# Kernel optimization log

Hardware: AMD Instinct MI355X
Metric: run time of the kernel (lower is better)

The kernel has to match this reference:

```python
import jax, jax.numpy as jnp
import numpy as np
from jax import lax

T_DATA = 20000
E_NO = 2000
I_NO = 500
SUB_NO = 16
SYN_B = 3
HID = 256
T_SYN = 200
T_ENC = 80


def _causal_conv(x, kern):
    # x: [T, S] per-subunit drive; kern: [S, K] causal kernels (index = lag)
    S, K = kern.shape
    lhs = jnp.pad(x.T, ((0, 0), (K - 1, 0)))[None]        # [1, S, T+K-1]
    rhs = kern[:, ::-1][:, None, :]                        # flip then correlate == torch conv1d path
    out = lax.conv_general_dilated(lhs, rhs, (1,), 'VALID', feature_group_count=S)
    return out[0].T                                        # [T, S]


def setup_inputs() -> dict:
    key = jax.random.key(0)
    ks = jax.random.split(key, 16)
    V_in = jax.random.normal(ks[0], (T_DATA,), jnp.float32) * 5.0 - 69.0
    S_e = jax.random.bernoulli(ks[1], 0.02, (T_DATA, E_NO)).astype(jnp.float32)
    S_i = jax.random.bernoulli(ks[2], 0.02, (T_DATA, I_NO)).astype(jnp.float32)
    # synapse -> subunit one-hot assignment matrices [sub_no, n_syn]
    C_syn_e = jax.nn.one_hot(jax.random.randint(ks[3], (E_NO,), 0, SUB_NO), SUB_NO, dtype=jnp.float32).T
    C_syn_i = jax.nn.one_hot(jax.random.randint(ks[4], (I_NO,), 0, SUB_NO), SUB_NO, dtype=jnp.float32).T
    # parameters, initialized exactly as in __init__
    K_syn = jnp.stack([jnp.full((SUB_NO, SYN_B), 0.04),
                       jnp.full((SUB_NO, SYN_B), -0.02),
                       jnp.full((SUB_NO, SYN_B), 0.02)], axis=-1)          # [sub, B, 3]
    tau_syn = jnp.tile((jnp.arange(SYN_B, dtype=jnp.float32) + 1.6)[:, None], (1, 3))  # [B, 3]
    delta_syn = jnp.full((SUB_NO, 2), 2.0, jnp.float32)
    enc_bias = jnp.zeros((SUB_NO - 1,), jnp.float32)
    W_in = 2 * T_ENC - 1

    def lin(k, fan_out, fan_in):
        kw, kb = jax.random.split(k)
        s = 1.0 / np.sqrt(fan_in)
        return (jax.random.uniform(kw, (fan_out, fan_in), jnp.float32, -s, s),
                jax.random.uniform(kb, (fan_out,), jnp.float32, -s, s))

    W1, b1 = lin(ks[5], HID, W_in)
    W2, b2 = lin(ks[6], HID, HID)
    W3, b3 = lin(ks[7], HID, HID)
    W4, b4 = lin(ks[8], SUB_NO - 1, HID)
    a1 = jnp.float32(0.25)
    a2 = jnp.float32(0.25)
    a3 = jnp.float32(0.25)
    return dict(V_in=V_in, S_e=S_e, S_i=S_i, C_syn_e=C_syn_e, C_syn_i=C_syn_i,
                K_syn=K_syn, tau_syn=tau_syn, delta_syn=delta_syn, enc_bias=enc_bias,
                W1=W1, b1=b1, a1=a1, W2=W2, b2=b2, a2=a2, W3=W3, b3=b3, a3=a3,
                W4=W4, b4=b4)


def reference(V_in, S_e, S_i, C_syn_e, C_syn_i, K_syn, tau_syn, delta_syn, enc_bias,
              W1, b1, a1, W2, b2, a2, W3, b3, a3, W4, b4):
    T = V_in.shape[0]
    # ---- spike_convolve, fully vectorized over (subunit, basis) ----
    t = jnp.arange(T_SYN, dtype=V_in.dtype)                 # [T_syn]
    d = jnp.exp(delta_syn)                                   # [sub, 2]
    te = jnp.maximum(t[None, :] - d[:, 0:1], 0.0)            # [sub, T_syn]
    ti = jnp.maximum(t[None, :] - d[:, 1:2], 0.0)
    tau = jnp.exp(tau_syn)                                   # [B, 3]
    tte = te[:, None, :] / tau[None, :, 0, None]             # [sub, B, T_syn]
    tti = ti[:, None, :] / tau[None, :, 1, None]
    ker_e = jnp.einsum('sbt,sb->st', tte * jnp.exp(-tte), K_syn[:, :, 0])
    ker_i = jnp.einsum('sbt,sb->st', tti * jnp.exp(-tti), K_syn[:, :, 1])
    in_e = S_e @ C_syn_e.T                                   # [T, sub]
    in_i = S_i @ C_syn_i.T
    S_conv = _causal_conv(in_e, ker_e) + _causal_conv(in_i, ker_i)   # [T, sub]
    # ---- encode: batched sliding-window MLP (replaces per-timestep loop) ----
    W = 2 * T_ENC - 1
    Vpad = jnp.zeros((T + W,), V_in.dtype).at[T_ENC - 1:T_ENC - 1 + T].set(V_in)
    idx = jnp.arange(T)[:, None] + jnp.arange(W)[None, :]    # [T, W]
    win = Vpad[idx]                                          # [T, W]
    prelu = lambda x, a: jnp.where(x >= 0, x, a * x)
    h = prelu(win @ W1.T + b1, a1)
    h = prelu(h @ W2.T + b2, a2)
    h = prelu(h @ W3.T + b3, a3)
    nn_out = h @ W4.T + b4                                   # [T, sub-1]
    return jax.nn.sigmoid(nn_out + S_conv[:, 1:] + enc_bias)
```

## Files before the change

kernel.cpp:

```cpp
#include <hip/hip_runtime.h>
#include <cstdint>
#include <cstddef>

#define T_DATA 20000
#define E_NO 2000
#define I_NO 500
#define SUB_NO 16
#define HID 256
#define T_SYN 200
#define T_ENC 80
#define W_IN 159

typedef __attribute__((ext_vector_type(8))) __bf16 bf16x8;
typedef __attribute__((ext_vector_type(8))) short short8;
typedef __attribute__((ext_vector_type(4))) float floatx4;
typedef __attribute__((ext_vector_type(4))) unsigned int uint4v;
typedef __attribute__((ext_vector_type(2))) unsigned int uint2v;

__device__ __forceinline__ float bf2f(unsigned short u) {
    union { unsigned int i; float f; } v; v.i = ((unsigned int)u) << 16; return v.f;
}
__device__ __forceinline__ unsigned short f2bf(float f) {
    union { float f; unsigned int i; } v; v.f = f;
    unsigned int r = v.i + 0x7FFFu + ((v.i >> 16) & 1u);
    return (unsigned short)(r >> 16);
}
__device__ __forceinline__ float inload(const void* p, int i, int isbf) {
    return isbf ? bf2f(((const unsigned short*)p)[i]) : ((const float*)p)[i];
}

__device__ __forceinline__ int detect_bf(const void* Se, int* sfl) {
    if (threadIdx.x == 0) *sfl = 0;
    __syncthreads();
    const unsigned int* w = (const unsigned int*)Se;
    int la = 0;
    #pragma unroll
    for (int i = 0; i < 4; i++)
        la |= (w[i * 256 + threadIdx.x] & 0xFFFFu) ? 1 : 0;
    if (la) atomicOr(sfl, 1);
    __syncthreads();
    return *sfl;
}

#define OFF_KERE   16u
#define OFF_KERI   12816u
#define OFF_SHE    25616u
#define OFF_SHI    33616u
#define OFF_W1H    35616u
#define OFF_W1L    117536u
#define OFF_W2H    199456u
#define OFF_W2L    330528u
#define OFF_W3H    461600u
#define OFF_W3L    592672u
#define OFF_W4H    723744u
#define OFF_W4L    731936u
#define OFF_INE    740128u
#define OFF_INI    1060128u

__global__ void k_tables(const void* Se, const void* Ksyn, const void* tau_syn, const void* dly,
                         const void* Ce, const void* Ci,
                         float* ker_e, float* ker_i, unsigned char* sh_e, unsigned char* sh_i) {
    __shared__ int sfl;
    int f = detect_bf(Se, &sfl);
    int id = blockIdx.x * 256 + threadIdx.x;
    if (id < 6400) {
        int c = id < 3200 ? 0 : 1;
        int q = id - c * 3200;
        int s = q / 200, j = q - s * 200;
        float d = expf(inload(dly, s * 2 + c, f));
        float tt = fmaxf((float)j - d, 0.0f);
        float acc = 0.f;
        #pragma unroll
        for (int b = 0; b < 3; b++) {
            float tau = expf(inload(tau_syn, b * 3 + c, f));
            float x = tt / tau;
            acc += x * expf(-x) * inload(Ksyn, (s * 3 + b) * 3 + c, f);
        }
        (c == 0 ? ker_e : ker_i)[s * 200 + j] = acc;
    } else if (id < 8400) {
        int e = id - 6400;
        int a = 0;
        for (int s = 0; s < 16; s++) if (inload(Ce, s * E_NO + e, f) > 0.5f) a = s;
        sh_e[e] = (unsigned char)(a * 8);
    } else if (id < 8900) {
        int e = id - 8400;
        int a = 0;
        for (int s = 0; s < 16; s++) if (inload(Ci, s * I_NO + e, f) > 0.5f) a = s;
        sh_i[e] = (unsigned char)(a * 8);
    }
}

__device__ __forceinline__ void acc_slot(unsigned int b, unsigned int sh,
                                         unsigned long long& lo, unsigned long long& hi) {
    unsigned int up = sh >> 6;
    unsigned int s6 = sh & 63;
    lo += (unsigned long long)(b & (up ^ 1u)) << s6;
    hi += (unsigned long long)(b & up) << s6;
}

__global__ void __launch_bounds__(256) k_spikes(const void* Se, const void* Si,
                         const unsigned char* sh_e, const unsigned char* sh_i,
                         const void* W1, const void* W2, const void* W3, const void* W4,
                         unsigned char* in_e, unsigned char* in_i,
                         unsigned short* W1h, unsigned short* W1l,
                         unsigned short* W2h, unsigned short* W2l,
                         unsigned short* W3h, unsigned short* W3l,
                         unsigned short* W4h, unsigned short* W4l) {
    __shared__ int sfl;
    __shared__ __align__(8) unsigned char she[E_NO];
    __shared__ __align__(8) unsigned char shi[I_NO];
    for (int i = threadIdx.x; i < E_NO / 4; i += 256)
        ((unsigned int*)she)[i] = ((const unsigned int*)sh_e)[i];
    for (int i = threadIdx.x; i < I_NO / 4; i += 256)
        ((unsigned int*)shi)[i] = ((const unsigned int*)sh_i)[i];
    int f = detect_bf(Se, &sfl);
    int lane = threadIdx.x & 63;
    int wave = threadIdx.x >> 6;
    int t = blockIdx.x * 4 + wave;
    unsigned long long e0 = 0, e1 = 0, i0 = 0, i1 = 0;
    if (f) {
        const uint4v* re = (const uint4v*)((const unsigned short*)Se + (size_t)t * E_NO);
        #pragma unroll
        for (int it = 0; it < 4; it++) {
            int c = it * 64 + lane;
            if (c < 250) {
                uint4v v = re[c];
                unsigned long long q = *(const unsigned long long*)&she[c * 8];
                #pragma unroll
                for (int w = 0; w < 4; w++) {
                    unsigned int x = v[w];
                    acc_slot((x >> 7) & 1u,  (unsigned int)(q >> (16 * w)) & 0xFFu, e0, e1);
                    acc_slot((x >> 23) & 1u, (unsigned int)(q >> (16 * w + 8)) & 0xFFu, e0, e1);
                }
            }
        }
        const uint2v* ri = (const uint2v*)((const unsigned short*)Si + (size_t)t * I_NO);
        #pragma unroll
        for (int it = 0; it < 2; it++) {
            int c = it * 64 + lane;
            if (c < 125) {
                uint2v v = ri[c];
                unsigned int q = *(const unsigned int*)&shi[c * 4];
                #pragma unroll
                for (int w = 0; w < 2; w++) {
                    unsigned int x = v[w];
                    acc_slot((x >> 7) & 1u,  (q >> (16 * w)) & 0xFFu, i0, i1);
                    acc_slot((x >> 23) & 1u, (q >> (16 * w + 8)) & 0xFFu, i0, i1);
                }
            }
        }
    } else {
        const uint4v* re = (const uint4v*)((const float*)Se + (size_t)t * E_NO);
        #pragma unroll
        for (int it = 0; it < 8; it++) {
            int c = it * 64 + lane;
            if (c < 500) {
                uint4v v = re[c];
                unsigned int q = *(const unsigned int*)&she[c * 4];
                #pragma unroll
                for (int w = 0; w < 4; w++)
                    acc_slot((v[w] >> 23) & 1u, (q >> (8 * w)) & 0xFFu, e0, e1);
            }
        }
        const uint2v* ri = (const uint2v*)((const float*)Si + (size_t)t * I_NO);
        #pragma unroll
        for (int it = 0; it < 4; it++) {
            int c = it * 64 + lane;
            if (c < 250) {
                uint2v v = ri[c];
                unsigned int q = *(const unsigned short*)&shi[c * 2];
                #pragma unroll
                for (int w = 0; w < 2; w++)
                    acc_slot((v[w] >> 23) & 1u, (q >> (8 * w)) & 0xFFu, i0, i1);
            }
        }
    }
    for (int off = 32; off; off >>= 1) {
        e0 += __shfl_xor(e0, off);
        e1 += __shfl_xor(e1, off);
        i0 += __shfl_xor(i0, off);
        i1 += __shfl_xor(i1, off);
    }
    if (lane < 16) {
        unsigned long long a = (lane < 8) ? e0 : e1;
        in_e[(size_t)t * 16 + lane] = (unsigned char)((a >> ((lane & 7) * 8)) & 0xFF);
    } else if (lane < 32) {
        int s = lane - 16;
        unsigned long long a = (s < 8) ? i0 : i1;
        in_i[(size_t)t * 16 + s] = (unsigned char)((a >> ((s & 7) * 8)) & 0xFF);
    }
    if (blockIdx.x < 688) {
        int q = blockIdx.x * 256 + threadIdx.x;
        if (q < 40960) {
            int j = q & 7, l = (q >> 3) & 63, r = q >> 9;
            int ks = r % 5, tile = r / 5;
            int n = tile * 16 + (l & 15);
            int k = ks * 32 + (l >> 4) * 8 + j;
            float v = (k < W_IN) ? inload(W1, n * W_IN + k, f) : 0.f;
            unsigned short hi = f2bf(v);
            W1h[q] = hi;
            W1l[q] = f2bf(v - bf2f(hi));
        } else if (q < 106496) {
            int p = q - 40960;
            int j = p & 7, l = (p >> 3) & 63, r = p >> 9;
            int ks = r & 7, tile = r >> 3;
            int n = tile * 16 + (l & 15);
            int k = ks * 32 + (l >> 4) * 8 + j;
            float v = inload(W2, n * 256 + k, f);
            unsigned short hi = f2bf(v);
            W2h[p] = hi;
            W2l[p] = f2bf(v - bf2f(hi));
        } else if (q < 172032) {
            int p = q - 106496;
            int j = p & 7, l = (p >> 3) & 63, r = p >> 9;
            int ks = r & 7, tile = r >> 3;
            int n = tile * 16 + (l & 15);
            int k = ks * 32 + (l >> 4) * 8 + j;
            float v = inload(W3, n * 256 + k, f);
            unsigned short hi = f2bf(v);
            W3h[p] = hi;
            W3l[p] = f2bf(v - bf2f(hi));
        } else {
            int p = q - 172032;
            int j = p & 7, l = (p >> 3) & 63, ks = p >> 9;
            int lm = l & 15, quad = l >> 4;
            float v = 0.f;
            if (lm < 15) v = inload(W4, lm * 256 + ks * 32 + quad * 8 + j, f);
            unsigned short hi = f2bf(v);
            W4h[p] = hi;
            W4l[p] = f2bf(v - bf2f(hi));
        }
    }
}

template<bool BF>
__device__ __forceinline__ void mlp_body(
    const void* V,
    const unsigned short* W1h, const unsigned short* W1l, const void* b1, const void* a1p,
    const unsigned short* W2h, const unsigned short* W2l, const void* b2, const void* a2p,
    const unsigned short* W3h, const unsigned short* W3l, const void* b3, const void* a3p,
    const unsigned short* W4h, const unsigned short* W4l, const void* b4,
    const void* encb, const float* Sc, void* out,
    unsigned short* Ahi, unsigned short* Alo,
    const bf16x8 (&Bh1)[5][4])
{
    int tid = threadIdx.x;
    int lane = tid & 63, wave = tid >> 6;
    int lm = lane & 15, quad = lane >> 4;
    int t0 = blockIdx.x * 64;

    auto ld = [&](const void* p, int i) -> float {
        return BF ? bf2f(((const unsigned short*)p)[i]) : ((const float*)p)[i];
    };
    auto boff1 = [&](int ks, int nt) { return (size_t)((((wave * 4 + nt) * 5 + ks) * 64 + lane) << 3); };
    auto boff  = [&](int ks, int nt) { return (size_t)((((wave * 4 + nt) * 8 + ks) * 64 + lane) << 3); };

    for (int idx = tid; idx < 64 * 160; idx += 256) {
        int m = idx / 160, k = idx - m * 160;
        int tg = t0 + m + k - (T_ENC - 1);
        float v = 0.f;
        if (k < W_IN && tg >= 0 && tg < T_DATA) v = ld(V, tg);
        unsigned short hi = f2bf(v);
        int col = (((k >> 3) ^ (m & 31)) << 3) | (k & 7);
        Ahi[m * 256 + col] = hi;
        if (!BF) Alo[m * 256 + col] = f2bf(v - bf2f(hi));
    }
    __syncthreads();

    floatx4 acc[4][4];
    auto aoff = [&](int mt, int ks) {
        int arow = mt * 16 + lm;
        return arow * 256 + ((((ks << 2) | quad) ^ (arow & 31)) << 3);
    };

    auto epi = [&](const void* bias, float alpha) {
        __syncthreads();
        #pragma unroll
        for (int mt = 0; mt < 4; mt++) {
            #pragma unroll
            for (int nt = 0; nt < 4; nt++) {
                int cn = wave * 64 + nt * 16 + lm;
                float bb = ld(bias, cn);
                #pragma unroll
                for (int j = 0; j < 4; j++) {
                    int row = mt * 16 + quad * 4 + j;
                    float h = acc[mt][nt][j] + bb;
                    h = (h >= 0.f) ? h : alpha * h;
                    unsigned short hi = f2bf(h);
                    int col = (((cn >> 3) ^ (row & 31)) << 3) | (cn & 7);
                    Ahi[row * 256 + col] = hi;
                    if (!BF) Alo[row * 256 + col] = f2bf(h - bf2f(hi));
                }
            }
        }
        __syncthreads();
    };

    floatx4 z = {0.f, 0.f, 0.f, 0.f};
    {
        #pragma unroll
        for (int mt = 0; mt < 4; mt++)
            #pragma unroll
            for (int nt = 0; nt < 4; nt++) acc[mt][nt] = z;
        if (BF) {
            #pragma unroll
            for (int ks = 0; ks < 5; ks++) {
                bf16x8 a[4];
                #pragma unroll
                for (int mt = 0; mt < 4; mt++) a[mt] = *(const bf16x8*)&Ahi[aoff(mt, ks)];
                #pragma unroll
                for (int nt = 0; nt < 4; nt++)
                    #pragma unroll
                    for (int mt = 0; mt < 4; mt++)
                        acc[mt][nt] = __builtin_amdgcn_mfma_f32_16x16x32_bf16(a[mt], Bh1[ks][nt], acc[mt][nt], 0, 0, 0);
            }
        } else {
            #pragma unroll
            for (int ks = 0; ks < 5; ks++) {
                bf16x8 ah[4], al[4];
                #pragma unroll
                for (int mt = 0; mt < 4; mt++) {
                    ah[mt] = *(const bf16x8*)&Ahi[aoff(mt, ks)];
                    al[mt] = *(const bf16x8*)&Alo[aoff(mt, ks)];
                }
                #pragma unroll
                for (int nt = 0; nt < 4; nt++) {
                    bf16x8 bh = Bh1[ks][nt];
                    bf16x8 bl = *(const bf16x8*)(W1l + boff1(ks, nt));
                    #pragma unroll
                    for (int mt = 0; mt < 4; mt++) {
                        acc[mt][nt] = __builtin_amdgcn_mfma_f32_16x16x32_bf16(ah[mt], bh, acc[mt][nt], 0, 0, 0);
                        acc[mt][nt] = __builtin_amdgcn_mfma_f32_16x16x32_bf16(al[mt], bh, acc[mt][nt], 0, 0, 0);
                        acc[mt][nt] = __builtin_amdgcn_mfma_f32_16x16x32_bf16(ah[mt], bl, acc[mt][nt], 0, 0, 0);
                    }
                }
            }
        }
        epi(b1, ld(a1p, 0));
    }
    const unsigned short* Whs[2] = {W2h, W3h};
    const unsigned short* Wls[2] = {W2l, W3l};
    const void* bs[2] = {b2, b3};
    const void* as_[2] = {a2p, a3p};
    for (int l = 0; l < 2; l++) {
        #pragma unroll
        for (int mt = 0; mt < 4; mt++)
            #pragma unroll
            for (int nt = 0; nt < 4; nt++) acc[mt][nt] = z;
        const unsigned short* Wh = Whs[l];
        const unsigned short* Wl = Wls[l];
        if (BF) {
            bf16x8 Bh[8][4];
            #pragma unroll
            for (int ks = 0; ks < 8; ks++)
                #pragma unroll
                for (int nt = 0; nt < 4; nt++)
                    Bh[ks][nt] = *(const bf16x8*)(Wh + boff(ks, nt));
            #pragma unroll
            for (int ks = 0; ks < 8; ks++) {
                bf16x8 a[4];
                #pragma unroll
                for (int mt = 0; mt < 4; mt++) a[mt] = *(const bf16x8*)&Ahi[aoff(mt, ks)];
                #pragma unroll
                for (int nt = 0; nt < 4; nt++)
                    #pragma unroll
                    for (int mt = 0; mt < 4; mt++)
                        acc[mt][nt] = __builtin_amdgcn_mfma_f32_16x16x32_bf16(a[mt], Bh[ks][nt], acc[mt][nt], 0, 0, 0);
            }
        } else {
            #pragma unroll
            for (int ks = 0; ks < 8; ks++) {
                bf16x8 ah[4], al[4];
                #pragma unroll
                for (int mt = 0; mt < 4; mt++) {
                    ah[mt] = *(const bf16x8*)&Ahi[aoff(mt, ks)];
                    al[mt] = *(const bf16x8*)&Alo[aoff(mt, ks)];
                }
                #pragma unroll
                for (int nt = 0; nt < 4; nt++) {
                    bf16x8 bh = *(const bf16x8*)(Wh + boff(ks, nt));
                    bf16x8 bl = *(const bf16x8*)(Wl + boff(ks, nt));
                    #pragma unroll
                    for (int mt = 0; mt < 4; mt++) {
                        acc[mt][nt] = __builtin_amdgcn_mfma_f32_16x16x32_bf16(ah[mt], bh, acc[mt][nt], 0, 0, 0);
                        acc[mt][nt] = __builtin_amdgcn_mfma_f32_16x16x32_bf16(al[mt], bh, acc[mt][nt], 0, 0, 0);
                        acc[mt][nt] = __builtin_amdgcn_mfma_f32_16x16x32_bf16(ah[mt], bl, acc[mt][nt], 0, 0, 0);
                    }
                }
            }
        }
        epi(bs[l], ld(as_[l], 0));
    }
    {
        int mt = wave;
        floatx4 a4 = z;
        #pragma unroll
        for (int ks = 0; ks < 8; ks++) {
            bf16x8 ah = *(const bf16x8*)&Ahi[aoff(mt, ks)];
            bf16x8 bh = *(const bf16x8*)(W4h + (size_t)((ks * 64 + lane) << 3));
            a4 = __builtin_amdgcn_mfma_f32_16x16x32_bf16(ah, bh, a4, 0, 0, 0);
            if (!BF) {
                bf16x8 al = *(const bf16x8*)&Alo[aoff(mt, ks)];
                bf16x8 bl = *(const bf16x8*)(W4l + (size_t)((ks * 64 + lane) << 3));
                a4 = __builtin_amdgcn_mfma_f32_16x16x32_bf16(al, bh, a4, 0, 0, 0);
                a4 = __builtin_amdgcn_mfma_f32_16x16x32_bf16(ah, bl, a4, 0, 0, 0);
            }
        }
        if (lm < 15) {
            float bb = ld(b4, lm) + ld(encb, lm);
            #pragma unroll
            for (int j = 0; j < 4; j++) {
                int row = mt * 16 + quad * 4 + j;
                int t = t0 + row;
                if (t < T_DATA) {
                    float x = a4[j] + bb + Sc[row * 16 + lm + 1];
                    x = fminf(fmaxf(x, -40.f), 40.f);
                    float sg = 1.f / (1.f + expf(-x));
                    if (BF) ((unsigned short*)out)[(size_t)t * 15 + lm] = f2bf(sg);
                    else    ((float*)out)[(size_t)t * 15 + lm] = sg;
                }
            }
        }
    }
}

__global__ void __launch_bounds__(256, 2) k_convmlp(
    const void* Se, const void* V,
    const unsigned char* in_e, const unsigned char* in_i,
    const float* ker_e, const float* ker_i,
    const unsigned short* W1h, const unsigned short* W1l, const void* b1, const void* a1p,
    const unsigned short* W2h, const unsigned short* W2l, const void* b2, const void* a2p,
    const unsigned short* W3h, const unsigned short* W3l, const void* b3, const void* a3p,
    const unsigned short* W4h, const unsigned short* W4l, const void* b4,
    const void* encb, void* out) {
    __shared__ __align__(16) unsigned char smem[65536];
    __shared__ __align__(16) float Sc[64 * 16];
    __shared__ int sfl;

    float* se = (float*)smem;
    float* si = se + 263 * 17;
    float* ke = si + 263 * 17;
    float* ki = ke + 16 * 201;

    int lane = threadIdx.x & 63, wave = threadIdx.x >> 6;

    bf16x8 Bh1[5][4];
    #pragma unroll
    for (int ks = 0; ks < 5; ks++)
        #pragma unroll
        for (int nt = 0; nt < 4; nt++)
            Bh1[ks][nt] = *(const bf16x8*)(W1h + (size_t)((((wave * 4 + nt) * 5 + ks) * 64 + lane) << 3));

    int t0 = blockIdx.x * 64;
    for (int idx = threadIdx.x; idx < 263 * 4; idx += 256) {
        int r = idx >> 2, wi = idx & 3;
        int t = t0 - 199 + r;
        unsigned int ve = 0, vi = 0;
        if (t >= 0 && t < T_DATA) {
            ve = ((const unsigned int*)in_e)[t * 4 + wi];
            vi = ((const unsigned int*)in_i)[t * 4 + wi];
        }
        #pragma unroll
        for (int b = 0; b < 4; b++) {
            se[r * 17 + wi * 4 + b] = (float)((ve >> (8 * b)) & 0xFF);
            si[r * 17 + wi * 4 + b] = (float)((vi >> (8 * b)) & 0xFF);
        }
    }
    for (int idx = threadIdx.x; idx < 3200; idx += 256) {
        int s2 = idx / 200, j = idx - s2 * 200;
        ke[s2 * 201 + j] = ker_e[idx];
        ki[s2 * 201 + j] = ker_i[idx];
    }
    int f = detect_bf(Se, &sfl);

    {
        int s = threadIdx.x & 15, g4 = (threadIdx.x >> 4) * 4;
        float a0 = 0.f, a1 = 0.f, a2 = 0.f, a3 = 0.f;
        float w0 = se[(g4 + 199) * 17 + s], w1 = se[(g4 + 200) * 17 + s];
        float w2 = se[(g4 + 201) * 17 + s], w3 = se[(g4 + 202) * 17 + s];
        float x0 = si[(g4 + 199) * 17 + s], x1 = si[(g4 + 200) * 17 + s];
        float x2 = si[(g4 + 201) * 17 + s], x3 = si[(g4 + 202) * 17 + s];
        #pragma unroll 4
        for (int j = 0; j < 200; j++) {
            float kej = ke[s * 201 + j];
            float kij = ki[s * 201 + j];
            a0 += w0 * kej + x0 * kij;
            a1 += w1 * kej + x1 * kij;
            a2 += w2 * kej + x2 * kij;
            a3 += w3 * kej + x3 * kij;
            int lr = g4 + 198 - j; lr = lr < 0 ? 0 : lr;
            float nw = se[lr * 17 + s], nx = si[lr * 17 + s];
            w3 = w2; w2 = w1; w1 = w0; w0 = nw;
            x3 = x2; x2 = x1; x1 = x0; x0 = nx;
        }
        Sc[(g4 + 0) * 16 + s] = a0;
        Sc[(g4 + 1) * 16 + s] = a1;
        Sc[(g4 + 2) * 16 + s] = a2;
        Sc[(g4 + 3) * 16 + s] = a3;
    }
    __syncthreads();

    unsigned short* Ahi = (unsigned short*)smem;
    unsigned short* Alo = Ahi + 64 * 256;
    if (f)
        mlp_body<true>(V, W1h, W1l, b1, a1p, W2h, W2l, b2, a2p, W3h, W3l, b3, a3p,
                       W4h, W4l, b4, encb, Sc, out, Ahi, Alo, Bh1);
    else
        mlp_body<false>(V, W1h, W1l, b1, a1p, W2h, W2l, b2, a2p, W3h, W3l, b3, a3p,
                        W4h, W4l, b4, encb, Sc, out, Ahi, Alo, Bh1);
}

extern "C" void kernel_launch(void* const* d_in, const int* in_sizes, int n_in,
                              void* d_out, int out_size, void* d_ws, size_t ws_size,
                              hipStream_t stream) {
    const void* V    = d_in[0];
    const void* Se   = d_in[1];
    const void* Si   = d_in[2];
    const void* Ce   = d_in[3];
    const void* Ci   = d_in[4];
    const void* Ksyn = d_in[5];
    const void* tau  = d_in[6];
    const void* dly  = d_in[7];
    const void* encb = d_in[8];
    const void* W1   = d_in[9];
    const void* b1   = d_in[10];
    const void* a1   = d_in[11];
    const void* W2   = d_in[12];
    const void* b2   = d_in[13];
    const void* a2   = d_in[14];
    const void* W3   = d_in[15];
    const void* b3   = d_in[16];
    const void* a3   = d_in[17];
    const void* W4   = d_in[18];
    const void* b4   = d_in[19];

    char* w = (char*)d_ws;
    float* ker_e = (float*)(w + OFF_KERE);
    float* ker_i = (float*)(w + OFF_KERI);
    unsigned char* sh_e = (unsigned char*)(w + OFF_SHE);
    unsigned char* sh_i = (unsigned char*)(w + OFF_SHI);
    unsigned short* W1h = (unsigned short*)(w + OFF_W1H);
    unsigned short* W1l = (unsigned short*)(w + OFF_W1L);
    unsigned short* W2h = (unsigned short*)(w + OFF_W2H);
    unsigned short* W2l = (unsigned short*)(w + OFF_W2L);
    unsigned short* W3h = (unsigned short*)(w + OFF_W3H);
    unsigned short* W3l = (unsigned short*)(w + OFF_W3L);
    unsigned short* W4h = (unsigned short*)(w + OFF_W4H);
    unsigned short* W4l = (unsigned short*)(w + OFF_W4L);
    unsigned char* in_e = (unsigned char*)(w + OFF_INE);
    unsigned char* in_i = (unsigned char*)(w + OFF_INI);

    k_tables<<<35, 256, 0, stream>>>(Se, Ksyn, tau, dly, Ce, Ci,
                                     ker_e, ker_i, sh_e, sh_i);
    k_spikes<<<5000, 256, 0, stream>>>(Se, Si, sh_e, sh_i, W1, W2, W3, W4,
                                       in_e, in_i,
                                       W1h, W1l, W2h, W2l, W3h, W3l, W4h, W4l);
    k_convmlp<<<313, 256, 0, stream>>>(Se, V, in_e, in_i, ker_e, ker_i,
                                       W1h, W1l, b1, a1, W2h, W2l, b2, a2,
                                       W3h, W3l, b3, a3, W4h, W4l, b4,
                                       encb, d_out);
}
```

Before: 355.4 us.

## Split conv by excitatory/inhibitory stream with 8-row register blocking and bf16 staging

The causal convolution stage now gives each half of the block one input stream (excitatory or inhibitory). Each thread computes 8 consecutive outputs instead of 4, so every kernel-tap load from shared memory is reused across more accumulators and the per-tap shared-memory reads drop. The two partial results go into a doubled Sc buffer and are summed in the final epilogue. Spike counts are staged as bf16, which is exact for small integers, to halve the LDS footprint. The bf16 MLP layers 2-3 also load W in two halves instead of all 32 fragments at once, to lower register pressure.

New measurement: 357.0 us. No clear change (+0.5%).

```diff
diff --git a/kernel.cpp b/kernel.cpp
--- a/kernel.cpp
+++ b/kernel.cpp
@@ -350,22 +350,26 @@
         const unsigned short* Wh = Whs[l];
         const unsigned short* Wl = Wls[l];
         if (BF) {
-            bf16x8 Bh[8][4];
-            #pragma unroll
-            for (int ks = 0; ks < 8; ks++)
-                #pragma unroll
-                for (int nt = 0; nt < 4; nt++)
-                    Bh[ks][nt] = *(const bf16x8*)(Wh + boff(ks, nt));
-            #pragma unroll
-            for (int ks = 0; ks < 8; ks++) {
-                bf16x8 a[4];
-                #pragma unroll
-                for (int mt = 0; mt < 4; mt++) a[mt] = *(const bf16x8*)&Ahi[aoff(mt, ks)];
-                #pragma unroll
-                for (int nt = 0; nt < 4; nt++)
+            #pragma unroll
+            for (int half = 0; half < 2; half++) {
+                bf16x8 Bh[4][4];
+                #pragma unroll
+                for (int c = 0; c < 4; c++)
                     #pragma unroll
-                    for (int mt = 0; mt < 4; mt++)
-                        acc[mt][nt] = __builtin_amdgcn_mfma_f32_16x16x32_bf16(a[mt], Bh[ks][nt], acc[mt][nt], 0, 0, 0);
+                    for (int nt = 0; nt < 4; nt++)
+                        Bh[c][nt] = *(const bf16x8*)(Wh + boff(half * 4 + c, nt));
+                #pragma unroll
+                for (int c = 0; c < 4; c++) {
+                    int ks = half * 4 + c;
+                    bf16x8 a[4];
+                    #pragma unroll
+                    for (int mt = 0; mt < 4; mt++) a[mt] = *(const bf16x8*)&Ahi[aoff(mt, ks)];
+                    #pragma unroll
+                    for (int nt = 0; nt < 4; nt++)
+                        #pragma unroll
+                        for (int mt = 0; mt < 4; mt++)
+                            acc[mt][nt] = __builtin_amdgcn_mfma_f32_16x16x32_bf16(a[mt], Bh[c][nt], acc[mt][nt], 0, 0, 0);
+                }
             }
         } else {
             #pragma unroll
@@ -413,7 +417,7 @@
                 int row = mt * 16 + quad * 4 + j;
                 int t = t0 + row;
                 if (t < T_DATA) {
-                    float x = a4[j] + bb + Sc[row * 16 + lm + 1];
+                    float x = a4[j] + bb + Sc[row * 16 + lm + 1] + Sc[1024 + row * 16 + lm + 1];
                     x = fminf(fmaxf(x, -40.f), 40.f);
                     float sg = 1.f / (1.f + expf(-x));
                     if (BF) ((unsigned short*)out)[(size_t)t * 15 + lm] = f2bf(sg);
@@ -434,15 +438,17 @@
     const unsigned short* W4h, const unsigned short* W4l, const void* b4,
     const void* encb, void* out) {
     __shared__ __align__(16) unsigned char smem[65536];
-    __shared__ __align__(16) float Sc[64 * 16];
+    __shared__ __align__(16) float Sc[2 * 64 * 16];
     __shared__ int sfl;
 
-    float* se = (float*)smem;
-    float* si = se + 263 * 17;
-    float* ke = si + 263 * 17;
-    float* ki = ke + 16 * 201;
-
-    int lane = threadIdx.x & 63, wave = threadIdx.x >> 6;
+    unsigned short* se16 = (unsigned short*)smem;
+    unsigned short* si16 = se16 + 4472;
+    float* kef = (float*)(smem + 17888);
+    float* kif = kef + 16 * 201;
+
+    int tid = threadIdx.x;
+    int lane = tid & 63, wave = tid >> 6;
+    int t0 = blockIdx.x * 64;
 
     bf16x8 Bh1[5][4];
     #pragma unroll
@@ -451,8 +457,7 @@
         for (int nt = 0; nt < 4; nt++)
             Bh1[ks][nt] = *(const bf16x8*)(W1h + (size_t)((((wave * 4 + nt) * 5 + ks) * 64 + lane) << 3));
 
-    int t0 = blockIdx.x * 64;
-    for (int idx = threadIdx.x; idx < 263 * 4; idx += 256) {
+    for (int idx = tid; idx < 263 * 4; idx += 256) {
         int r = idx >> 2, wi = idx & 3;
         int t = t0 - 199 + r;
         unsigned int ve = 0, vi = 0;
@@ -462,41 +467,43 @@
         }
         #pragma unroll
         for (int b = 0; b < 4; b++) {
-            se[r * 17 + wi * 4 + b] = (float)((ve >> (8 * b)) & 0xFF);
-            si[r * 17 + wi * 4 + b] = (float)((vi >> (8 * b)) & 0xFF);
-        }
-    }
-    for (int idx = threadIdx.x; idx < 3200; idx += 256) {
+            se16[r * 17 + wi * 4 + b] = f2bf((float)((ve >> (8 * b)) & 0xFF));
+            si16[r * 17 + wi * 4 + b] = f2bf((float)((vi >> (8 * b)) & 0xFF));
+        }
+    }
+    for (int idx = tid; idx < 3200; idx += 256) {
         int s2 = idx / 200, j = idx - s2 * 200;
-        ke[s2 * 201 + j] = ker_e[idx];
-        ki[s2 * 201 + j] = ker_i[idx];
+        kef[s2 * 201 + j] = ker_e[idx];
+        kif[s2 * 201 + j] = ker_i[idx];
     }
     int f = detect_bf(Se, &sfl);
 
     {
-        int s = threadIdx.x & 15, g4 = (threadIdx.x >> 4) * 4;
-        float a0 = 0.f, a1 = 0.f, a2 = 0.f, a3 = 0.f;
-        float w0 = se[(g4 + 199) * 17 + s], w1 = se[(g4 + 200) * 17 + s];
-        float w2 = se[(g4 + 201) * 17 + s], w3 = se[(g4 + 202) * 17 + s];
-        float x0 = si[(g4 + 199) * 17 + s], x1 = si[(g4 + 200) * 17 + s];
-        float x2 = si[(g4 + 201) * 17 + s], x3 = si[(g4 + 202) * 17 + s];
-        #pragma unroll 4
+        int arr = tid >> 7;
+        int g8 = ((tid >> 4) & 7) * 8;
+        int s  = tid & 15;
+        const unsigned short* src = arr ? si16 : se16;
+        const float* kf = arr ? kif : kef;
+        float w[8], acc8[8];
+        #pragma unroll
+        for (int i = 0; i < 8; i++) {
+            w[i] = bf2f(src[(g8 + i + 199) * 17 + s]);
+            acc8[i] = 0.f;
+        }
+        #pragma unroll 8
         for (int j = 0; j < 200; j++) {
-            float kej = ke[s * 201 + j];
-            float kij = ki[s * 201 + j];
-            a0 += w0 * kej + x0 * kij;
-            a1 += w1 * kej + x1 * kij;
-            a2 += w2 * kej + x2 * kij;
-            a3 += w3 * kej + x3 * kij;
-            int lr = g4 + 198 - j; lr = lr < 0 ? 0 : lr;
-            float nw = se[lr * 17 + s], nx = si[lr * 17 + s];
-            w3 = w2; w2 = w1; w1 = w0; w0 = nw;
-            x3 = x2; x2 = x1; x1 = x0; x0 = nx;
-        }
-        Sc[(g4 + 0) * 16 + s] = a0;
-        Sc[(g4 + 1) * 16 + s] = a1;
-        Sc[(g4 + 2) * 16 + s] = a2;
-        Sc[(g4 + 3) * 16 + s] = a3;
+            float kj = kf[s * 201 + j];
+            #pragma unroll
+            for (int i = 0; i < 8; i++) acc8[i] += w[i] * kj;
+            int lr = g8 + 198 - j; lr = lr < 0 ? 0 : lr;
+            float nv = bf2f(src[lr * 17 + s]);
+            #pragma unroll
+            for (int i = 7; i > 0; i--) w[i] = w[i - 1];
+            w[0] = nv;
+        }
+        #pragma unroll
+        for (int i = 0; i < 8; i++)
+            Sc[arr * 1024 + (g8 + i) * 16 + s] = acc8[i];
     }
     __syncthreads();
 
```
